# Performance work log

Measured on AMD Instinct MI355X. Metric: run time of the kernel, lower is better.

The kernel has to match this reference:

```python
import jax, jax.numpy as jnp
import numpy as np
from jax import lax

B_SZ, L, D, N = 4, 2048, 768, 16


def setup_inputs() -> dict:
    key = jax.random.key(0)
    ks = jax.random.split(key, 8)
    x = jax.random.normal(ks[0], (B_SZ, L, D), dtype=jnp.float32)
    # A_log init: log(repeat(arange(1, N+1), 'n -> d n'))
    A_log = jnp.log(jnp.tile(jnp.arange(1, N + 1, dtype=jnp.float32), (D, 1)))  # (D, N)
    sD = 1.0 / np.sqrt(D)
    Wb = jax.random.normal(ks[1], (N, D), dtype=jnp.float32) * sD
    bb = jax.random.normal(ks[2], (N,), dtype=jnp.float32) * sD
    Wc = jax.random.normal(ks[3], (N, D), dtype=jnp.float32) * sD
    bc = jax.random.normal(ks[4], (N,), dtype=jnp.float32) * sD
    W1 = jax.random.normal(ks[5], (1, D), dtype=jnp.float32) * sD
    b1 = jnp.zeros((1,), dtype=jnp.float32)
    Wd = jax.random.normal(ks[6], (D, 1), dtype=jnp.float32)
    bd = jax.random.normal(ks[7], (D,), dtype=jnp.float32)
    return {"x": x, "A_log": A_log, "Wb": Wb, "bb": bb, "Wc": Wc, "bc": bc,
            "W1": W1, "b1": b1, "Wd": Wd, "bd": bd}


def reference(x, A_log, Wb, bb, Wc, bc, W1, b1, Wd, bd):
    # x: (b, l, d)
    A = -jnp.exp(A_log)                                   # (d, n)
    Bp = x @ Wb.T + bb                                    # (b, l, n)
    C = x @ Wc.T + bc                                     # (b, l, n)
    s1 = x @ W1.T + b1                                    # (b, l, 1)
    delta = jax.nn.softplus(s1 @ Wd.T + bd)               # (b, l, d)
    deltaA = jnp.exp(jnp.einsum('bld,dn->bldn', delta, A))          # (b, l, d, n)
    deltaB_u = jnp.einsum('bld,bln,bld->bldn', delta, Bp, x)        # (b, l, d, n)

    def step(h, inputs):
        dA, dBu, c = inputs                               # (b,d,n),(b,d,n),(b,n)
        h = dA * h + dBu
        y = jnp.einsum('bdn,bn->bd', h, c)
        return h, y

    b, l, d = x.shape
    n = A_log.shape[1]
    h0 = jnp.zeros((b, d, n), dtype=x.dtype)
    _, ys = lax.scan(step, h0, (jnp.moveaxis(deltaA, 1, 0),
                                jnp.moveaxis(deltaB_u, 1, 0),
                                jnp.moveaxis(C, 1, 0)))
    return jnp.moveaxis(ys, 0, 1)                          # (b, l, d)
```

## Files before the change

### kernel.cpp

```cpp
#include <hip/hip_runtime.h>
#include <math.h>

#define B_SZ 4
#define LSEQ 2048
#define DDIM 768
#define NST  16
#define NROW (B_SZ * LSEQ)
#define NJ   33

#define NC   128
#define CS   (LSEQ / NC)

#define KSPL 32
#define KCH  (DDIM / KSPL)

__global__ __launch_bounds__(256) void proj_part_kernel(
    const float* __restrict__ x,
    const float* __restrict__ Wb, const float* __restrict__ Wc,
    const float* __restrict__ W1, float* __restrict__ part)
{
    const int row = blockIdx.x * 256 + threadIdx.x;
    const int s = blockIdx.y;
    const int k0 = s * KCH;

    float4 xv[6];
    const float* xp = x + (size_t)row * DDIM + k0;
    #pragma unroll
    for (int q = 0; q < 6; ++q) xv[q] = *(const float4*)(xp + q * 4);

    float acc[NJ];
    #pragma unroll
    for (int j = 0; j < NJ; ++j) {
        const float* wrow = (j < 16) ? (Wb + j * DDIM)
                          : (j < 32) ? (Wc + (j - 16) * DDIM)
                                     : W1;
        const float* wk = wrow + k0;
        float a = 0.f;
        #pragma unroll
        for (int q = 0; q < 6; ++q) {
            a = fmaf(xv[q].x, wk[q * 4 + 0], a);
            a = fmaf(xv[q].y, wk[q * 4 + 1], a);
            a = fmaf(xv[q].z, wk[q * 4 + 2], a);
            a = fmaf(xv[q].w, wk[q * 4 + 3], a);
        }
        acc[j] = a;
    }
    #pragma unroll
    for (int j = 0; j < NJ; ++j)
        part[((size_t)s * NJ + j) * NROW + row] = acc[j];
}

__global__ __launch_bounds__(256) void proj_reduce_kernel(
    const float* __restrict__ part,
    const float* __restrict__ bb, const float* __restrict__ bc,
    const float* __restrict__ b1,
    float* __restrict__ Bp, float* __restrict__ Cc, float* __restrict__ s1)
{
    const int idx = blockIdx.x * 256 + threadIdx.x;
    if (idx >= NJ * NROW) return;
    const int j = idx / NROW;
    const int row = idx % NROW;
    float a = 0.f;
    #pragma unroll 8
    for (int s = 0; s < KSPL; ++s)
        a += part[((size_t)s * NJ + j) * NROW + row];
    if (j < 16)      Bp[(size_t)row * NST + j] = a + bb[j];
    else if (j < 32) Cc[(size_t)row * NST + (j - 16)] = a + bc[j - 16];
    else             s1[row] = a + b1[0];
}

__device__ __forceinline__ float softplus_f(float z) {
    float t = __expf(-fabsf(z));
    return fmaxf(z, 0.f) + __logf(1.f + t);
}

__device__ __forceinline__ void powers16(float p, float* e) {
    e[0] = p;      e[1] = p * p;      e[2] = e[1] * p;   e[3] = e[1] * e[1];
    e[4] = e[3] * p;  e[5] = e[3] * e[1];  e[6] = e[3] * e[2];  e[7] = e[3] * e[3];
    e[8] = e[7] * p;  e[9] = e[7] * e[1];  e[10] = e[7] * e[2]; e[11] = e[7] * e[3];
    e[12] = e[7] * e[4]; e[13] = e[7] * e[5]; e[14] = e[7] * e[6]; e[15] = e[7] * e[7];
}

__device__ __forceinline__ bool a_structured(const float* acoef) {
    bool st = true;
    #pragma unroll
    for (int n = 0; n < NST; ++n)
        st = st && (fabsf(acoef[n] - (float)(n + 1) * acoef[0]) <= 1e-5f * fabsf(acoef[n]));
    return __all(st) != 0;
}

__global__ __launch_bounds__(256) void pass1_kernel(
    const float* __restrict__ x, const float* __restrict__ A_log,
    const float* __restrict__ Wd, const float* __restrict__ bd,
    const float* __restrict__ Bp, const float* __restrict__ s1,
    float* __restrict__ Ssum, float* __restrict__ Q)
{
    const int tid = threadIdx.x;
    const int d = blockIdx.x * 256 + tid;
    const int c = blockIdx.y, b = blockIdx.z;
    const int rowbase = b * LSEQ + c * CS;

    const float wd = Wd[d], bdv = bd[d];
    float acoef[NST];
    #pragma unroll
    for (int n = 0; n < NST; ++n) acoef[n] = -__expf(A_log[d * NST + n]);
    const float a0 = acoef[0];
    const bool structured = a_structured(acoef);

    const float4* B4 = (const float4*)(Bp + (size_t)rowbase * NST);
    const float* s1p = s1 + rowbase;
    const float* xp = x + (size_t)rowbase * DDIM + d;

    float h[NST];
    #pragma unroll
    for (int n = 0; n < NST; ++n) h[n] = 0.f;
    float S = 0.f;

    if (structured) {
        #pragma unroll 4
        for (int l = 0; l < CS; ++l) {
            const float delta = softplus_f(fmaf(s1p[l], wd, bdv));
            S += delta;
            float e[NST];
            powers16(__expf(delta * a0), e);
            const float dx = delta * xp[(size_t)l * DDIM];
            const float4 b0 = B4[l * 4 + 0], b1v = B4[l * 4 + 1];
            const float4 b2 = B4[l * 4 + 2], b3v = B4[l * 4 + 3];
            const float bv[NST] = {b0.x, b0.y, b0.z, b0.w, b1v.x, b1v.y, b1v.z, b1v.w,
                                   b2.x, b2.y, b2.z, b2.w, b3v.x, b3v.y, b3v.z, b3v.w};
            #pragma unroll
            for (int n = 0; n < NST; ++n) h[n] = fmaf(e[n], h[n], dx * bv[n]);
        }
    } else {
        #pragma unroll 4
        for (int l = 0; l < CS; ++l) {
            const float delta = softplus_f(fmaf(s1p[l], wd, bdv));
            S += delta;
            float e[NST];
            #pragma unroll
            for (int n = 0; n < NST; ++n) e[n] = __expf(delta * acoef[n]);
            const float dx = delta * xp[(size_t)l * DDIM];
            const float4 b0 = B4[l * 4 + 0], b1v = B4[l * 4 + 1];
            const float4 b2 = B4[l * 4 + 2], b3v = B4[l * 4 + 3];
            const float bv[NST] = {b0.x, b0.y, b0.z, b0.w, b1v.x, b1v.y, b1v.z, b1v.w,
                                   b2.x, b2.y, b2.z, b2.w, b3v.x, b3v.y, b3v.z, b3v.w};
            #pragma unroll
            for (int n = 0; n < NST; ++n) h[n] = fmaf(e[n], h[n], dx * bv[n]);
        }
    }
    Ssum[((size_t)b * NC + c) * DDIM + d] = S;
    const size_t gbase = (((size_t)b * NC + c) * DDIM + d) * NST;
    float4* Q4 = (float4*)(Q + gbase);
    #pragma unroll
    for (int q = 0; q < 4; ++q)
        Q4[q] = make_float4(h[q * 4], h[q * 4 + 1], h[q * 4 + 2], h[q * 4 + 3]);
}

#define CPG (NC / 4)
__global__ __launch_bounds__(256) void combine_kernel(
    const float* __restrict__ A_log,
    const float* __restrict__ Ssum, const float* __restrict__ Q,
    float* __restrict__ Hin)
{
    const int gidx = blockIdx.x * 256 + threadIdx.x;
    const int lane = threadIdx.x & 63;
    const int rlow = gidx & 15;
    const int g = (gidx >> 4) & 3;
    const int hi = gidx >> 6;
    const int pairIdx = hi * 16 + rlow;
    const int b = pairIdx / (DDIM * NST);
    const int r = pairIdx % (DDIM * NST);
    const int d = r >> 4;
    const float acoef = -__expf(A_log[r]);
    const int c0 = g * CPG;

    float eq[CPG], qq[CPG];
    #pragma unroll
    for (int ci = 0; ci < CPG; ++ci) {
        const size_t base = (size_t)(b * NC + c0 + ci);
        eq[ci] = __expf(acoef * Ssum[base * DDIM + d]);
        qq[ci] = Q[base * (DDIM * NST) + r];
    }
    float E = 1.f, H = 0.f;
    #pragma unroll
    for (int ci = 0; ci < CPG; ++ci) { H = fmaf(eq[ci], H, qq[ci]); E *= eq[ci]; }

    float oE = __shfl_up(E, 16, 64);
    float oH = __shfl_up(H, 16, 64);
    if (lane >= 16) { H = fmaf(E, oH, H); E *= oE; }
    oE = __shfl_up(E, 32, 64);
    oH = __shfl_up(H, 32, 64);
    if (lane >= 32) { H = fmaf(E, oH, H); E *= oE; }

    float hin = __shfl_up(H, 16, 64);
    if (g == 0) hin = 0.f;

    float h = hin;
    #pragma unroll
    for (int ci = 0; ci < CPG; ++ci) {
        const size_t base = (size_t)(b * NC + c0 + ci);
        Hin[base * (DDIM * NST) + r] = h;
        h = fmaf(eq[ci], h, qq[ci]);
    }
}

__global__ __launch_bounds__(256) void pass2_kernel(
    const float* __restrict__ x, const float* __restrict__ A_log,
    const float* __restrict__ Wd, const float* __restrict__ bd,
    const float* __restrict__ Bp, const float* __restrict__ Cc,
    const float* __restrict__ s1, const float* __restrict__ Hin,
    float* __restrict__ out)
{
    const int tid = threadIdx.x;
    const int d = blockIdx.x * 256 + tid;
    const int c = blockIdx.y, b = blockIdx.z;
    const int rowbase = b * LSEQ + c * CS;

    const float wd = Wd[d], bdv = bd[d];
    float acoef[NST];
    #pragma unroll
    for (int n = 0; n < NST; ++n) acoef[n] = -__expf(A_log[d * NST + n]);
    const float a0 = acoef[0];
    const bool structured = a_structured(acoef);

    const float4* B4 = (const float4*)(Bp + (size_t)rowbase * NST);
    const float4* C4 = (const float4*)(Cc + (size_t)rowbase * NST);
    const float* s1p = s1 + rowbase;
    const float* xp = x + (size_t)rowbase * DDIM + d;
    float* yp = out + (size_t)rowbase * DDIM + d;

    float h[NST];
    const size_t gbase = (((size_t)b * NC + c) * DDIM + d) * NST;
    const float4* H4 = (const float4*)(Hin + gbase);
    #pragma unroll
    for (int q = 0; q < 4; ++q) {
        const float4 hv = H4[q];
        h[q * 4] = hv.x; h[q * 4 + 1] = hv.y; h[q * 4 + 2] = hv.z; h[q * 4 + 3] = hv.w;
    }

    if (structured) {
        #pragma unroll 4
        for (int l = 0; l < CS; ++l) {
            const float delta = softplus_f(fmaf(s1p[l], wd, bdv));
            float e[NST];
            powers16(__expf(delta * a0), e);
            const float dx = delta * xp[(size_t)l * DDIM];
            const float4 b0 = B4[l * 4 + 0], b1v = B4[l * 4 + 1];
            const float4 b2 = B4[l * 4 + 2], b3v = B4[l * 4 + 3];
            const float4 c0 = C4[l * 4 + 0], c1v = C4[l * 4 + 1];
            const float4 c2 = C4[l * 4 + 2], c3v = C4[l * 4 + 3];
            const float bv[NST] = {b0.x, b0.y, b0.z, b0.w, b1v.x, b1v.y, b1v.z, b1v.w,
                                   b2.x, b2.y, b2.z, b2.w, b3v.x, b3v.y, b3v.z, b3v.w};
            const float cv[NST] = {c0.x, c0.y, c0.z, c0.w, c1v.x, c1v.y, c1v.z, c1v.w,
                                   c2.x, c2.y, c2.z, c2.w, c3v.x, c3v.y, c3v.z, c3v.w};
            float y = 0.f;
            #pragma unroll
            for (int n = 0; n < NST; ++n) {
                h[n] = fmaf(e[n], h[n], dx * bv[n]);
                y = fmaf(h[n], cv[n], y);
            }
            yp[(size_t)l * DDIM] = y;
        }
    } else {
        #pragma unroll 4
        for (int l = 0; l < CS; ++l) {
            const float delta = softplus_f(fmaf(s1p[l], wd, bdv));
            float e[NST];
            #pragma unroll
            for (int n = 0; n < NST; ++n) e[n] = __expf(delta * acoef[n]);
            const float dx = delta * xp[(size_t)l * DDIM];
            const float4 b0 = B4[l * 4 + 0], b1v = B4[l * 4 + 1];
            const float4 b2 = B4[l * 4 + 2], b3v = B4[l * 4 + 3];
            const float4 c0 = C4[l * 4 + 0], c1v = C4[l * 4 + 1];
            const float4 c2 = C4[l * 4 + 2], c3v = C4[l * 4 + 3];
            const float bv[NST] = {b0.x, b0.y, b0.z, b0.w, b1v.x, b1v.y, b1v.z, b1v.w,
                                   b2.x, b2.y, b2.z, b2.w, b3v.x, b3v.y, b3v.z, b3v.w};
            const float cv[NST] = {c0.x, c0.y, c0.z, c0.w, c1v.x, c1v.y, c1v.z, c1v.w,
                                   c2.x, c2.y, c2.z, c2.w, c3v.x, c3v.y, c3v.z, c3v.w};
            float y = 0.f;
            #pragma unroll
            for (int n = 0; n < NST; ++n) {
                h[n] = fmaf(e[n], h[n], dx * bv[n]);
                y = fmaf(h[n], cv[n], y);
            }
            yp[(size_t)l * DDIM] = y;
        }
    }
}

extern "C" void kernel_launch(void* const* d_in, const int* in_sizes, int n_in,
                              void* d_out, int out_size, void* d_ws, size_t ws_size,
                              hipStream_t stream) {
    const float* x     = (const float*)d_in[0];
    const float* A_log = (const float*)d_in[1];
    const float* Wb    = (const float*)d_in[2];
    const float* bb    = (const float*)d_in[3];
    const float* Wc    = (const float*)d_in[4];
    const float* bc    = (const float*)d_in[5];
    const float* W1    = (const float*)d_in[6];
    const float* b1    = (const float*)d_in[7];
    const float* Wd    = (const float*)d_in[8];
    const float* bd    = (const float*)d_in[9];
    float* out = (float*)d_out;

    float* ws = (float*)d_ws;
    const size_t partN = (size_t)KSPL * NJ * NROW;
    const size_t BpN = (size_t)NROW * NST;
    const size_t s1N = (size_t)NROW;
    const size_t sN  = (size_t)B_SZ * NC * DDIM;
    const size_t agg = (size_t)B_SZ * NC * DDIM * NST;

    float* part = ws;
    float* Bp   = part + partN;
    float* Cc   = Bp + BpN;
    float* s1   = Cc + BpN;
    float* Ssum = s1 + s1N;
    float* Q    = Ssum + sN;
    float* Hin  = Q + agg;

    dim3 gproj(NROW / 256, KSPL);
    proj_part_kernel<<<gproj, 256, 0, stream>>>(x, Wb, Wc, W1, part);
    proj_reduce_kernel<<<(NJ * NROW + 255) / 256, 256, 0, stream>>>(part, bb, bc, b1, Bp, Cc, s1);

    dim3 gscan(DDIM / 256, NC, B_SZ);
    pass1_kernel<<<gscan, 256, 0, stream>>>(x, A_log, Wd, bd, Bp, s1, Ssum, Q);

    combine_kernel<<<(B_SZ * DDIM * NST * 4) / 256, 256, 0, stream>>>(A_log, Ssum, Q, Hin);

    pass2_kernel<<<gscan, 256, 0, stream>>>(x, A_log, Wd, bd, Bp, Cc, s1, Hin, out);
}
```

Measured before the change: 155.7 us.

## Fuse all five stages into one cooperative persistent kernel with grid syncs

Replaces the five kernel launches with one cooperative kernel of 768 blocks that runs the projection partials, the reduction, the chunk scan, the cross-chunk combine and the output pass, separated by grid.sync. It also switches to 64 chunks of 32 steps and a 24-way K split, and keeps each chunk's x values in registers so the second pass does not reload them. The goal is to remove launch gaps and cut repeated traffic. In exchange it adds grid-wide barrier cost, more register pressure from the 32-entry x array, and less parallelism per phase. If the cooperative launch fails, the old multi-kernel path is used.

```diff
diff --git a/kernel.cpp b/kernel.cpp
--- a/kernel.cpp
+++ b/kernel.cpp
@@ -1,5 +1,8 @@
 #include <hip/hip_runtime.h>
+#include <hip/hip_cooperative_groups.h>
 #include <math.h>
+
+namespace cg = cooperative_groups;
 
 #define B_SZ 4
 #define LSEQ 2048
@@ -8,11 +11,273 @@
 #define NROW (B_SZ * LSEQ)
 #define NJ   33
 
+#define FNB  768
+#define FNT  (FNB * 256)
+#define FNC  64
+#define FCS  (LSEQ / FNC)
+#define FCPG (FNC / 4)
+#define PKS  24
+#define PKC  (DDIM / PKS)
+
 #define NC   128
 #define CS   (LSEQ / NC)
-
 #define KSPL 32
 #define KCH  (DDIM / KSPL)
+
+__device__ __forceinline__ float softplus_f(float z) {
+    float t = __expf(-fabsf(z));
+    return fmaxf(z, 0.f) + __logf(1.f + t);
+}
+
+__device__ __forceinline__ void powers16(float p, float* e) {
+    e[0] = p;      e[1] = p * p;      e[2] = e[1] * p;   e[3] = e[1] * e[1];
+    e[4] = e[3] * p;  e[5] = e[3] * e[1];  e[6] = e[3] * e[2];  e[7] = e[3] * e[3];
+    e[8] = e[7] * p;  e[9] = e[7] * e[1];  e[10] = e[7] * e[2]; e[11] = e[7] * e[3];
+    e[12] = e[7] * e[4]; e[13] = e[7] * e[5]; e[14] = e[7] * e[6]; e[15] = e[7] * e[7];
+}
+
+__device__ __forceinline__ bool a_structured(const float* acoef) {
+    bool st = true;
+    #pragma unroll
+    for (int n = 0; n < NST; ++n)
+        st = st && (fabsf(acoef[n] - (float)(n + 1) * acoef[0]) <= 1e-5f * fabsf(acoef[n]));
+    return __all(st) != 0;
+}
+
+__global__ __launch_bounds__(256, 3) void fused_kernel(
+    const float* __restrict__ x, const float* __restrict__ A_log,
+    const float* __restrict__ Wb, const float* __restrict__ bb,
+    const float* __restrict__ Wc, const float* __restrict__ bc,
+    const float* __restrict__ W1, const float* __restrict__ b1,
+    const float* __restrict__ Wd, const float* __restrict__ bd,
+    float* __restrict__ part, float* __restrict__ Bp, float* __restrict__ Cc,
+    float* __restrict__ s1, float* __restrict__ Ssum, float* __restrict__ Q,
+    float* __restrict__ Hin, float* __restrict__ out)
+{
+    cg::grid_group grid = cg::this_grid();
+    const int tid = threadIdx.x;
+    const int bx = blockIdx.x;
+    const int gidx = bx * 256 + tid;
+
+    {
+        const int row = gidx & (NROW - 1);
+        const int s = gidx >> 13;
+        const int k0 = s * PKC;
+        float4 xv[PKC / 4];
+        const float* xp0 = x + (size_t)row * DDIM + k0;
+        #pragma unroll
+        for (int q = 0; q < PKC / 4; ++q) xv[q] = *(const float4*)(xp0 + q * 4);
+        #pragma unroll
+        for (int j = 0; j < NJ; ++j) {
+            const float* wrow = (j < 16) ? (Wb + j * DDIM)
+                              : (j < 32) ? (Wc + (j - 16) * DDIM)
+                                         : W1;
+            const float* wk = wrow + k0;
+            float a = 0.f;
+            #pragma unroll
+            for (int q = 0; q < PKC / 4; ++q) {
+                a = fmaf(xv[q].x, wk[q * 4 + 0], a);
+                a = fmaf(xv[q].y, wk[q * 4 + 1], a);
+                a = fmaf(xv[q].z, wk[q * 4 + 2], a);
+                a = fmaf(xv[q].w, wk[q * 4 + 3], a);
+            }
+            part[((size_t)s * NJ + j) * NROW + row] = a;
+        }
+    }
+    grid.sync();
+
+    #pragma unroll
+    for (int it = 0; it < 2; ++it) {
+        const int idx = gidx + it * FNT;
+        if (idx < NJ * NROW) {
+            const int j = idx / NROW;
+            const int row = idx - j * NROW;
+            float a = 0.f;
+            #pragma unroll 8
+            for (int s = 0; s < PKS; ++s)
+                a += part[((size_t)s * NJ + j) * NROW + row];
+            if (j < 16)      Bp[(size_t)row * NST + j] = a + bb[j];
+            else if (j < 32) Cc[(size_t)row * NST + (j - 16)] = a + bc[j - 16];
+            else             s1[row] = a + b1[0];
+        }
+    }
+    grid.sync();
+
+    const int d  = (bx % 3) * 256 + tid;
+    const int c  = (bx / 3) & (FNC - 1);
+    const int b  = bx / (3 * FNC);
+    const int rowbase = b * LSEQ + c * FCS;
+
+    const float wd = Wd[d], bdv = bd[d];
+    float acoef[NST];
+    #pragma unroll
+    for (int n = 0; n < NST; ++n) acoef[n] = -__expf(A_log[d * NST + n]);
+    const float a0 = acoef[0];
+    const bool structured = a_structured(acoef);
+
+    const float4* B4 = (const float4*)(Bp + (size_t)rowbase * NST);
+    const float* s1p = s1 + rowbase;
+
+    float xfull[FCS];
+    {
+        const float* xp = x + (size_t)rowbase * DDIM + d;
+        #pragma unroll
+        for (int l = 0; l < FCS; ++l) xfull[l] = xp[(size_t)l * DDIM];
+    }
+
+    {
+        float h[NST];
+        #pragma unroll
+        for (int n = 0; n < NST; ++n) h[n] = 0.f;
+        float S = 0.f;
+
+        if (structured) {
+            #pragma unroll 4
+            for (int l = 0; l < FCS; ++l) {
+                const float delta = softplus_f(fmaf(s1p[l], wd, bdv));
+                S += delta;
+                float e[NST];
+                powers16(__expf(delta * a0), e);
+                const float dx = delta * xfull[l];
+                const float4 b0 = B4[l * 4 + 0], b1v = B4[l * 4 + 1];
+                const float4 b2 = B4[l * 4 + 2], b3v = B4[l * 4 + 3];
+                const float bv[NST] = {b0.x, b0.y, b0.z, b0.w, b1v.x, b1v.y, b1v.z, b1v.w,
+                                       b2.x, b2.y, b2.z, b2.w, b3v.x, b3v.y, b3v.z, b3v.w};
+                #pragma unroll
+                for (int n = 0; n < NST; ++n) h[n] = fmaf(e[n], h[n], dx * bv[n]);
+            }
+        } else {
+            #pragma unroll 4
+            for (int l = 0; l < FCS; ++l) {
+                const float delta = softplus_f(fmaf(s1p[l], wd, bdv));
+                S += delta;
+                float e[NST];
+                #pragma unroll
+                for (int n = 0; n < NST; ++n) e[n] = __expf(delta * acoef[n]);
+                const float dx = delta * xfull[l];
+                const float4 b0 = B4[l * 4 + 0], b1v = B4[l * 4 + 1];
+                const float4 b2 = B4[l * 4 + 2], b3v = B4[l * 4 + 3];
+                const float bv[NST] = {b0.x, b0.y, b0.z, b0.w, b1v.x, b1v.y, b1v.z, b1v.w,
+                                       b2.x, b2.y, b2.z, b2.w, b3v.x, b3v.y, b3v.z, b3v.w};
+                #pragma unroll
+                for (int n = 0; n < NST; ++n) h[n] = fmaf(e[n], h[n], dx * bv[n]);
+            }
+        }
+        Ssum[((size_t)b * FNC + c) * DDIM + d] = S;
+        const size_t gbase = (((size_t)b * FNC + c) * DDIM + d) * NST;
+        float4* Q4 = (float4*)(Q + gbase);
+        #pragma unroll
+        for (int q = 0; q < 4; ++q)
+            Q4[q] = make_float4(h[q * 4], h[q * 4 + 1], h[q * 4 + 2], h[q * 4 + 3]);
+    }
+    grid.sync();
+
+    {
+        const int lane = tid & 63;
+        const int rlow = gidx & 15;
+        const int g = (gidx >> 4) & 3;
+        const int hi = gidx >> 6;
+        const int pairIdx = hi * 16 + rlow;
+        const int bb_ = pairIdx / (DDIM * NST);
+        const int r = pairIdx % (DDIM * NST);
+        const int dd = r >> 4;
+        const float ac = -__expf(A_log[r]);
+        const int c0 = g * FCPG;
+
+        float eq[FCPG], qq[FCPG];
+        #pragma unroll
+        for (int ci = 0; ci < FCPG; ++ci) {
+            const size_t base = (size_t)(bb_ * FNC + c0 + ci);
+            eq[ci] = __expf(ac * Ssum[base * DDIM + dd]);
+            qq[ci] = Q[base * (DDIM * NST) + r];
+        }
+        float E = 1.f, H = 0.f;
+        #pragma unroll
+        for (int ci = 0; ci < FCPG; ++ci) { H = fmaf(eq[ci], H, qq[ci]); E *= eq[ci]; }
+
+        float oE = __shfl_up(E, 16, 64);
+        float oH = __shfl_up(H, 16, 64);
+        if (lane >= 16) { H = fmaf(E, oH, H); E *= oE; }
+        oE = __shfl_up(E, 32, 64);
+        oH = __shfl_up(H, 32, 64);
+        if (lane >= 32) { H = fmaf(E, oH, H); E *= oE; }
+
+        float hin = __shfl_up(H, 16, 64);
+        if (g == 0) hin = 0.f;
+
+        float h = hin;
+        #pragma unroll
+        for (int ci = 0; ci < FCPG; ++ci) {
+            const size_t base = (size_t)(bb_ * FNC + c0 + ci);
+            Hin[base * (DDIM * NST) + r] = h;
+            h = fmaf(eq[ci], h, qq[ci]);
+        }
+    }
+    grid.sync();
+
+    {
+        const float4* C4 = (const float4*)(Cc + (size_t)rowbase * NST);
+        float* yp = out + (size_t)rowbase * DDIM + d;
+
+        float h[NST];
+        const size_t gbase = (((size_t)b * FNC + c) * DDIM + d) * NST;
+        const float4* H4 = (const float4*)(Hin + gbase);
+        #pragma unroll
+        for (int q = 0; q < 4; ++q) {
+            const float4 hv = H4[q];
+            h[q * 4] = hv.x; h[q * 4 + 1] = hv.y; h[q * 4 + 2] = hv.z; h[q * 4 + 3] = hv.w;
+        }
+
+        if (structured) {
+            #pragma unroll 4
+            for (int l = 0; l < FCS; ++l) {
+                const float delta = softplus_f(fmaf(s1p[l], wd, bdv));
+                float e[NST];
+                powers16(__expf(delta * a0), e);
+                const float dx = delta * xfull[l];
+                const float4 b0 = B4[l * 4 + 0], b1v = B4[l * 4 + 1];
+                const float4 b2 = B4[l * 4 + 2], b3v = B4[l * 4 + 3];
+                const float4 c0v = C4[l * 4 + 0], c1v = C4[l * 4 + 1];
+                const float4 c2v = C4[l * 4 + 2], c3v = C4[l * 4 + 3];
+                const float bv[NST] = {b0.x, b0.y, b0.z, b0.w, b1v.x, b1v.y, b1v.z, b1v.w,
+                                       b2.x, b2.y, b2.z, b2.w, b3v.x, b3v.y, b3v.z, b3v.w};
+                const float cv[NST] = {c0v.x, c0v.y, c0v.z, c0v.w, c1v.x, c1v.y, c1v.z, c1v.w,
+                                       c2v.x, c2v.y, c2v.z, c2v.w, c3v.x, c3v.y, c3v.z, c3v.w};
+                float y = 0.f;
+                #pragma unroll
+                for (int n = 0; n < NST; ++n) {
+                    h[n] = fmaf(e[n], h[n], dx * bv[n]);
+                    y = fmaf(h[n], cv[n], y);
+                }
+                yp[(size_t)l * DDIM] = y;
+            }
+        } else {
+            #pragma unroll 4
+            for (int l = 0; l < FCS; ++l) {
+                const float delta = softplus_f(fmaf(s1p[l], wd, bdv));
+                float e[NST];
+                #pragma unroll
+                for (int n = 0; n < NST; ++n) e[n] = __expf(delta * acoef[n]);
+                const float dx = delta * xfull[l];
+                const float4 b0 = B4[l * 4 + 0], b1v = B4[l * 4 + 1];
+                const float4 b2 = B4[l * 4 + 2], b3v = B4[l * 4 + 3];
+                const float4 c0v = C4[l * 4 + 0], c1v = C4[l * 4 + 1];
+                const float4 c2v = C4[l * 4 + 2], c3v = C4[l * 4 + 3];
+                const float bv[NST] = {b0.x, b0.y, b0.z, b0.w, b1v.x, b1v.y, b1v.z, b1v.w,
+                                       b2.x, b2.y, b2.z, b2.w, b3v.x, b3v.y, b3v.z, b3v.w};
+                const float cv[NST] = {c0v.x, c0v.y, c0v.z, c0v.w, c1v.x, c1v.y, c1v.z, c1v.w,
+                                       c2v.x, c2v.y, c2v.z, c2v.w, c3v.x, c3v.y, c3v.z, c3v.w};
+                float y = 0.f;
+                #pragma unroll
+                for (int n = 0; n < NST; ++n) {
+                    h[n] = fmaf(e[n], h[n], dx * bv[n]);
+                    y = fmaf(h[n], cv[n], y);
+                }
+                yp[(size_t)l * DDIM] = y;
+            }
+        }
+    }
+}
 
 __global__ __launch_bounds__(256) void proj_part_kernel(
     const float* __restrict__ x,
@@ -22,12 +287,10 @@
     const int row = blockIdx.x * 256 + threadIdx.x;
     const int s = blockIdx.y;
     const int k0 = s * KCH;
-
     float4 xv[6];
     const float* xp = x + (size_t)row * DDIM + k0;
     #pragma unroll
     for (int q = 0; q < 6; ++q) xv[q] = *(const float4*)(xp + q * 4);
-
     float acc[NJ];
     #pragma unroll
     for (int j = 0; j < NJ; ++j) {
@@ -69,26 +332,6 @@
     else             s1[row] = a + b1[0];
 }
 
-__device__ __forceinline__ float softplus_f(float z) {
-    float t = __expf(-fabsf(z));
-    return fmaxf(z, 0.f) + __logf(1.f + t);
-}
-
-__device__ __forceinline__ void powers16(float p, float* e) {
-    e[0] = p;      e[1] = p * p;      e[2] = e[1] * p;   e[3] = e[1] * e[1];
-    e[4] = e[3] * p;  e[5] = e[3] * e[1];  e[6] = e[3] * e[2];  e[7] = e[3] * e[3];
-    e[8] = e[7] * p;  e[9] = e[7] * e[1];  e[10] = e[7] * e[2]; e[11] = e[7] * e[3];
-    e[12] = e[7] * e[4]; e[13] = e[7] * e[5]; e[14] = e[7] * e[6]; e[15] = e[7] * e[7];
-}
-
-__device__ __forceinline__ bool a_structured(const float* acoef) {
-    bool st = true;
-    #pragma unroll
-    for (int n = 0; n < NST; ++n)
-        st = st && (fabsf(acoef[n] - (float)(n + 1) * acoef[0]) <= 1e-5f * fabsf(acoef[n]));
-    return __all(st) != 0;
-}
-
 __global__ __launch_bounds__(256) void pass1_kernel(
     const float* __restrict__ x, const float* __restrict__ A_log,
     const float* __restrict__ Wd, const float* __restrict__ bd,
@@ -99,23 +342,19 @@
     const int d = blockIdx.x * 256 + tid;
     const int c = blockIdx.y, b = blockIdx.z;
     const int rowbase = b * LSEQ + c * CS;
-
     const float wd = Wd[d], bdv = bd[d];
     float acoef[NST];
     #pragma unroll
     for (int n = 0; n < NST; ++n) acoef[n] = -__expf(A_log[d * NST + n]);
     const float a0 = acoef[0];
     const bool structured = a_structured(acoef);
-
     const float4* B4 = (const float4*)(Bp + (size_t)rowbase * NST);
     const float* s1p = s1 + rowbase;
     const float* xp = x + (size_t)rowbase * DDIM + d;
-
     float h[NST];
     #pragma unroll
     for (int n = 0; n < NST; ++n) h[n] = 0.f;
     float S = 0.f;
-
     if (structured) {
         #pragma unroll 4
         for (int l = 0; l < CS; ++l) {
@@ -173,7 +412,6 @@
     const int d = r >> 4;
     const float acoef = -__expf(A_log[r]);
     const int c0 = g * CPG;
-
     float eq[CPG], qq[CPG];
     #pragma unroll
     for (int ci = 0; ci < CPG; ++ci) {
@@ -184,17 +422,14 @@
     float E = 1.f, H = 0.f;
     #pragma unroll
     for (int ci = 0; ci < CPG; ++ci) { H = fmaf(eq[ci], H, qq[ci]); E *= eq[ci]; }
-
     float oE = __shfl_up(E, 16, 64);
     float oH = __shfl_up(H, 16, 64);
     if (lane >= 16) { H = fmaf(E, oH, H); E *= oE; }
     oE = __shfl_up(E, 32, 64);
     oH = __shfl_up(H, 32, 64);
     if (lane >= 32) { H = fmaf(E, oH, H); E *= oE; }
-
     float hin = __shfl_up(H, 16, 64);
     if (g == 0) hin = 0.f;
-
     float h = hin;
     #pragma unroll
     for (int ci = 0; ci < CPG; ++ci) {
@@ -215,20 +450,17 @@
     const int d = blockIdx.x * 256 + tid;
     const int c = blockIdx.y, b = blockIdx.z;
     const int rowbase = b * LSEQ + c * CS;
-
     const float wd = Wd[d], bdv = bd[d];
     float acoef[NST];
     #pragma unroll
     for (int n = 0; n < NST; ++n) acoef[n] = -__expf(A_log[d * NST + n]);
     const float a0 = acoef[0];
     const bool structured = a_structured(acoef);
-
     const float4* B4 = (const float4*)(Bp + (size_t)rowbase * NST);
     const float4* C4 = (const float4*)(Cc + (size_t)rowbase * NST);
     const float* s1p = s1 + rowbase;
     const float* xp = x + (size_t)rowbase * DDIM + d;
     float* yp = out + (size_t)rowbase * DDIM + d;
-
     float h[NST];
     const size_t gbase = (((size_t)b * NC + c) * DDIM + d) * NST;
     const float4* H4 = (const float4*)(Hin + gbase);
@@ -237,7 +469,6 @@
         const float4 hv = H4[q];
         h[q * 4] = hv.x; h[q * 4 + 1] = hv.y; h[q * 4 + 2] = hv.z; h[q * 4 + 3] = hv.w;
     }
-
     if (structured) {
         #pragma unroll 4
         for (int l = 0; l < CS; ++l) {
@@ -318,14 +549,22 @@
     float* Q    = Ssum + sN;
     float* Hin  = Q + agg;
 
+    void* args[] = {(void*)&x, (void*)&A_log, (void*)&Wb, (void*)&bb,
+                    (void*)&Wc, (void*)&bc, (void*)&W1, (void*)&b1,
+                    (void*)&Wd, (void*)&bd,
+                    (void*)&part, (void*)&Bp, (void*)&Cc, (void*)&s1,
+                    (void*)&Ssum, (void*)&Q, (void*)&Hin, (void*)&out};
+    hipError_t err = hipLaunchCooperativeKernel((const void*)fused_kernel,
+                                                dim3(FNB), dim3(256),
+                                                args, 0, stream);
+    if (err == hipSuccess) return;
+    (void)hipGetLastError();
+
     dim3 gproj(NROW / 256, KSPL);
     proj_part_kernel<<<gproj, 256, 0, stream>>>(x, Wb, Wc, W1, part);
     proj_reduce_kernel<<<(NJ * NROW + 255) / 256, 256, 0, stream>>>(part, bb, bc, b1, Bp, Cc, s1);
-
     dim3 gscan(DDIM / 256, NC, B_SZ);
     pass1_kernel<<<gscan, 256, 0, stream>>>(x, A_log, Wd, bd, Bp, s1, Ssum, Q);
-
     combine_kernel<<<(B_SZ * DDIM * NST * 4) / 256, 256, 0, stream>>>(A_log, Ssum, Q, Hin);
-
     pass2_kernel<<<gscan, 256, 0, stream>>>(x, A_log, Wd, bd, Bp, Cc, s1, Hin, out);
 }
```

Measured after the change: 565.9 us. +263.6%, slower.
